# Kernel tuning notes

Hardware: AMD Instinct MI355X
Metric: run time of the kernel (lower is better)

Reference implementation:

```python
import jax, jax.numpy as jnp
import numpy as np

ALPHA = 0.2  # LeakyReLU negative slope
MASK_VAL = -9e15


def setup_inputs() -> dict:
    key = jax.random.key(0)
    k1, k2, k3, k4 = jax.random.split(key, 4)
    B, N, F_IN = 4, 2048, 256
    H, HD = 8, 32  # out_features = H*HD = 256
    x = jax.random.normal(k1, (B, N, F_IN), dtype=jnp.float32)
    adj = jax.random.randint(k2, (B, N, N), 0, 2, dtype=jnp.int32)
    W = jax.random.normal(k3, (H, F_IN, HD), dtype=jnp.float32) * (1.0 / np.sqrt(F_IN))
    a = jax.random.normal(k4, (H, 2 * HD, 1), dtype=jnp.float32) * 0.1
    return {"x": x, "adj": adj, "W": W, "a": a}


def reference(x, adj, W, a):
    # x: (B,N,F), W: (H,F,D), a: (H,2D,1)
    B, N, _ = x.shape
    H, _, D = W.shape
    Wh = jnp.einsum('bnf,hfd->bhnd', x, W)  # (B,H,N,D)
    # Split additive attention vector: cat([Wh_i, Wh_j]) @ a == Wh_i@a1 + Wh_j@a2
    a1 = a[:, :D, 0]   # (H,D)
    a2 = a[:, D:, 0]   # (H,D)
    s1 = jnp.einsum('bhnd,hd->bhn', Wh, a1)  # source scores
    s2 = jnp.einsum('bhnd,hd->bhn', Wh, a2)  # target scores
    e = jax.nn.leaky_relu(s1[:, :, :, None] + s2[:, :, None, :], negative_slope=ALPHA)  # (B,H,N,N)
    e = jnp.where(adj[:, None, :, :] == 0, MASK_VAL, e)
    attention = jax.nn.softmax(e, axis=-1)  # dropout skipped (eval mode)
    h = jnp.einsum('bhij,bhjd->bhid', attention, Wh)  # (B,H,N,D)
    h = jnp.transpose(h, (0, 2, 1, 3)).reshape(B, N, H * D)
    return jax.nn.elu(h)
```

## Files before the change

### kernel.cpp

```cpp
#include <hip/hip_runtime.h>
#include <hip/hip_bf16.h>

#define ALPHA 0.2f

typedef __attribute__((ext_vector_type(8))) short short8;
typedef __attribute__((ext_vector_type(8))) _Float16 h8;
typedef __attribute__((ext_vector_type(2))) _Float16 h2v;
typedef __attribute__((ext_vector_type(4))) float f32x4;

static constexpr int B = 4, N = 2048, F = 256, H = 8, D = 32;
static constexpr int SZ_X = B * N * F, SZ_ADJ = B * N * N, SZ_W = H * F * D, SZ_A = H * 2 * D;
static const float C1 = 1.4426950408889634f;
static const float C2 = ALPHA * 1.4426950408889634f;


__device__ __forceinline__ unsigned rne16(unsigned u) {
    return u + 0x7fffu + ((u >> 16) & 1u);
}
__device__ __forceinline__ unsigned pk_rne(float a, float b) {
    return __builtin_amdgcn_perm(rne16(__float_as_uint(b)),
                                 rne16(__float_as_uint(a)), 0x07060302u);
}
__device__ __forceinline__ unsigned h2mul(unsigned a, unsigned b) {
    h2v r = __builtin_bit_cast(h2v, a) * __builtin_bit_cast(h2v, b);
    return __builtin_bit_cast(unsigned, r);
}
__device__ __forceinline__ unsigned h2max(unsigned a, unsigned b) {
    h2v r = __builtin_elementwise_max(__builtin_bit_cast(h2v, a),
                                      __builtin_bit_cast(h2v, b));
    return __builtin_bit_cast(unsigned, r);
}

__global__ void k0_prep(const float* __restrict__ Wp, const float* __restrict__ ap,
                        unsigned short* __restrict__ WTbf, float* __restrict__ AF) {
    int bid = blockIdx.x;
    int h = bid >> 5, d = bid & 31;
    int f = threadIdx.x;
    WTbf[(h * D + d) * F + f] =
        (unsigned short)(rne16(__float_as_uint(Wp[(h * F + f) * D + d])) >> 16);
    if (d == 0 && f < 64) AF[h * 64 + f] = ap[h * 64 + f];
}

__global__ void kbit(const int* __restrict__ adj, unsigned long long* __restrict__ bm) {
    int wid = blockIdx.x * 4 + (threadIdx.x >> 6);
    int lane = threadIdx.x & 63;
    size_t base = (size_t)wid * 16;
#pragma unroll
    for (int s = 0; s < 16; s++) {
        size_t strip = base + s;
        int v = adj[strip * 64 + lane];
        unsigned long long m = __ballot(v != 0);
        if (lane == 0) bm[strip] = m;
    }
}

__global__ __launch_bounds__(256) void k12(const float* __restrict__ x,
                                           const unsigned short* __restrict__ WTbf,
                                           const float* __restrict__ AF,
                                           unsigned short* __restrict__ WHT,
                                           float* __restrict__ S1,
                                           _Float16* __restrict__ UH,
                                           _Float16* __restrict__ VH) {
    __shared__ unsigned short XA[16 * 264];
    __shared__ unsigned short WB[256 * 40];
    int bid = blockIdx.x;
    int b = bid >> 7;
    int n0 = (bid & 127) * 16;
    int t = threadIdx.x;
    int wave = t >> 6, lane = t & 63;
    int lm = lane & 15, lq = lane >> 4;

#pragma unroll
    for (int q = 0; q < 4; q++) {
        int idx = q * 256 + t;
        int row = idx >> 6, c16 = idx & 63;
        f32x4 v = *(const f32x4*)(x + (size_t)(b * N + n0 + row) * F + c16 * 4);
        unsigned* dst = (unsigned*)&XA[row * 264 + c16 * 4];
        dst[0] = pk_rne(v[0], v[1]);
        dst[1] = pk_rne(v[2], v[3]);
    }

    f32x4 acc[4] = {};
    for (int kc = 0; kc < 8; kc++) {
        __syncthreads();
#pragma unroll
        for (int q = 0; q < 4; q++) {
            int idx = q * 256 + t;
            int row = idx >> 2, c = idx & 3;
            short8 w = *(const short8*)(WTbf + row * 256 + kc * 32 + c * 8);
            *(short8*)&WB[row * 40 + c * 8] = w;
        }
        __syncthreads();
        short8 afr = *(const short8*)&XA[lm * 264 + kc * 32 + lq * 8];
#pragma unroll
        for (int c = 0; c < 4; c++) {
            short8 bfr = *(const short8*)&WB[(wave * 64 + c * 16 + lm) * 40 + lq * 8];
            acc[c] = __builtin_amdgcn_mfma_f32_16x16x32_bf16(afr, bfr, acc[c], 0, 0, 0);
        }
    }

#pragma unroll
    for (int c = 0; c < 4; c++) {
        int hd = wave * 64 + c * 16 + lm;
        unsigned short w0 = __builtin_bit_cast(unsigned short, (_Float16)acc[c][0]);
        unsigned short w1 = __builtin_bit_cast(unsigned short, (_Float16)acc[c][1]);
        unsigned short w2 = __builtin_bit_cast(unsigned short, (_Float16)acc[c][2]);
        unsigned short w3 = __builtin_bit_cast(unsigned short, (_Float16)acc[c][3]);
        uint2 pk;
        pk.x = (unsigned)w0 | ((unsigned)w1 << 16);
        pk.y = (unsigned)w2 | ((unsigned)w3 << 16);
        *(uint2*)&WHT[((size_t)b * 256 + hd) * 2048 + n0 + lq * 4] = pk;
    }
#pragma unroll
    for (int cp = 0; cp < 2; cp++) {
        int h = wave * 2 + cp;
        float a1l = AF[h * 64 + lm],      a1h = AF[h * 64 + 16 + lm];
        float a2l = AF[h * 64 + 32 + lm], a2h = AF[h * 64 + 48 + lm];
#pragma unroll
        for (int r = 0; r < 4; r++) {
            float s1p = acc[cp * 2][r] * a1l + acc[cp * 2 + 1][r] * a1h;
            float s2p = acc[cp * 2][r] * a2l + acc[cp * 2 + 1][r] * a2h;
#pragma unroll
            for (int off = 1; off <= 8; off <<= 1) {
                s1p += __shfl_xor(s1p, off);
                s2p += __shfl_xor(s2p, off);
            }
            if (lm == 0) {
                int bh = b * 8 + h, n = n0 + lq * 4 + r;
                S1[(size_t)bh * 2048 + n] = s1p;
                UH[(size_t)bh * 2048 + n] = (_Float16)exp2f(C1 * s2p);
                VH[(size_t)bh * 2048 + n] = (_Float16)exp2f(C2 * s2p);
            }
        }
    }
}

__global__ __launch_bounds__(512) void k3_attn(
    const unsigned* __restrict__ bm32,
    const unsigned short* __restrict__ WHT,
    const float* __restrict__ S1,
    const _Float16* __restrict__ UH, const _Float16* __restrict__ VH,
    float* __restrict__ out) {
    __shared__ unsigned short LW[256 * 136];
    __shared__ unsigned LM[16 * 66];
    __shared__ unsigned short LU[8 * 128];
    __shared__ unsigned short LV[8 * 128];

    int bid = blockIdx.x;
    int b = bid >> 7;
    int i0 = (bid & 127) * 16;
    int t = threadIdx.x;
    int wave = t >> 6, lane = t & 63;
    int h = wave;
    int bh = b * 8 + h;
    int irow = lane & 15, quad = lane >> 4;

    {
        int row = t >> 5, w0 = (t & 31) * 2;
        uint2 mv = *(const uint2*)(bm32 + ((size_t)(b * N + i0 + row)) * 64 + w0);
        LM[row * 66 + w0] = mv.x;
        LM[row * 66 + w0 + 1] = mv.y;
    }

    float s1i = S1[(size_t)bh * N + i0 + irow];
    unsigned short cw = __builtin_bit_cast(unsigned short, (_Float16)exp2f((C2 - C1) * s1i));
    unsigned ci2 = (unsigned)cw | ((unsigned)cw << 16);

    union { h8 v; unsigned u[4]; } ones;
    ones.u[0] = ones.u[1] = ones.u[2] = ones.u[3] = 0x3C003C00u;

    f32x4 acc0 = {0.f, 0.f, 0.f, 0.f};
    f32x4 acc1 = {0.f, 0.f, 0.f, 0.f};
    f32x4 accL = {0.f, 0.f, 0.f, 0.f};

    for (int cc = 0; cc < 16; cc++) {
        __syncthreads();
        const unsigned short* src = WHT + (size_t)b * 256 * 2048 + cc * 128;
#pragma unroll
        for (int q = 0; q < 8; q++) {
            int idx = q * 512 + t;
            int row = idx >> 4, u = idx & 15;
            short8 v = *(const short8*)(src + (size_t)row * 2048 + u * 8);
            *(short8*)&LW[row * 136 + u * 8] = v;
        }
        if (t < 256) {
            int which = t >> 7;
            int hh = (t & 127) >> 4, u16 = t & 15;
            const _Float16* s = (which ? VH : UH) + (size_t)(b * 8 + hh) * 2048 + cc * 128 + u16 * 8;
            short8 v = *(const short8*)s;
            unsigned short* dst = which ? LV : LU;
            *(short8*)&dst[hh * 128 + u16 * 8] = v;
        }
        __syncthreads();
#pragma unroll
        for (int g = 0; g < 4; g++) {
            unsigned mk = LM[irow * 66 + cc * 4 + g] >> (quad * 8);
            int jl = g * 32 + quad * 8;
            uint4 uw = *(const uint4*)&LU[h * 128 + jl];
            uint4 vw = *(const uint4*)&LV[h * 128 + jl];
            unsigned m0 = ((mk & 1u)   ? 0x3C00u : 0u) | ((mk & 2u)   ? 0x3C000000u : 0u);
            unsigned m1 = ((mk & 4u)   ? 0x3C00u : 0u) | ((mk & 8u)   ? 0x3C000000u : 0u);
            unsigned m2 = ((mk & 16u)  ? 0x3C00u : 0u) | ((mk & 32u)  ? 0x3C000000u : 0u);
            unsigned m3 = ((mk & 64u)  ? 0x3C00u : 0u) | ((mk & 128u) ? 0x3C000000u : 0u);
            union { h8 v; unsigned u[4]; } af;
            af.u[0] = h2mul(h2max(uw.x, h2mul(ci2, vw.x)), m0);
            af.u[1] = h2mul(h2max(uw.y, h2mul(ci2, vw.y)), m1);
            af.u[2] = h2mul(h2max(uw.z, h2mul(ci2, vw.z)), m2);
            af.u[3] = h2mul(h2max(uw.w, h2mul(ci2, vw.w)), m3);
            h8 bf0 = *(const h8*)&LW[(h * 32 + irow) * 136 + jl];
            h8 bf1 = *(const h8*)&LW[(h * 32 + 16 + irow) * 136 + jl];
            acc0 = __builtin_amdgcn_mfma_f32_16x16x32_f16(af.v, bf0, acc0, 0, 0, 0);
            acc1 = __builtin_amdgcn_mfma_f32_16x16x32_f16(af.v, bf1, acc1, 0, 0, 0);
            accL = __builtin_amdgcn_mfma_f32_16x16x32_f16(af.v, ones.v, accL, 0, 0, 0);
        }
    }
#pragma unroll
    for (int r = 0; r < 4; r++) {
        float lr = accL[r];
        float rin = 1.0f / (lr > 0.f ? lr : 1.f);
        float v0 = acc0[r] * rin;
        float v1 = acc1[r] * rin;
        v0 = v0 > 0.f ? v0 : __expf(v0) - 1.f;
        v1 = v1 > 0.f ? v1 : __expf(v1) - 1.f;
        size_t rowb = (size_t)(b * N + i0 + quad * 4 + r) * (H * D) + h * D;
        out[rowb + irow] = v0;
        out[rowb + 16 + irow] = v1;
    }
}

extern "C" void kernel_launch(void* const* d_in, const int* in_sizes, int n_in,
                              void* d_out, int out_size, void* d_ws, size_t ws_size,
                              hipStream_t stream) {
    const void *xP = nullptr, *adjP = nullptr, *WP = nullptr, *aP = nullptr;
    for (int i = 0; i < n_in; i++) {
        switch (in_sizes[i]) {
            case SZ_X:   xP = d_in[i]; break;
            case SZ_ADJ: adjP = d_in[i]; break;
            case SZ_W:   WP = d_in[i]; break;
            case SZ_A:   aP = d_in[i]; break;
            default: break;
        }
    }
    if (!xP || !adjP || !WP || !aP) { xP = d_in[0]; adjP = d_in[1]; WP = d_in[2]; aP = d_in[3]; }
    float* out = (float*)d_out;

    char* ws = (char*)d_ws;
    unsigned short* WTbf = (unsigned short*)(ws);
    float* AF  = (float*)(ws + 131072);
    float* S1  = (float*)(ws + 133120);
    _Float16* UH = (_Float16*)(ws + 395264);
    _Float16* VH = (_Float16*)(ws + 526336);
    unsigned short* WHT = (unsigned short*)(ws + 657408);
    unsigned long long* BM = (unsigned long long*)(ws + 4851712);

    k0_prep<<<256, 256, 0, stream>>>((const float*)WP, (const float*)aP, WTbf, AF);
    kbit<<<4096, 256, 0, stream>>>((const int*)adjP, BM);
    k12<<<512, 256, 0, stream>>>((const float*)xP, WTbf, AF, WHT, S1, UH, VH);
    k3_attn<<<512, 512, 0, stream>>>((const unsigned*)BM, WHT, S1, UH, VH, out);
}
```

Measured before the change: 164.5 us.

## Fuse adjacency bitmask build into attention kernel and use per-wave private LDS tiles

Removes the separate kbit kernel: each attention block now reads its 16 adjacency rows directly and ballots them into an LDS bitmask, avoiding a kernel launch and the bitmask round trip through global memory. The attention loop no longer uses block-wide barriers. Each wave loads only its own head's 32 WHT rows into a private LDS slice, and U/V values are read straight from global memory. Without barriers, waves can drift apart and overlap loads with MFMA work. The cost is that the adjacency read is now serialized at block start with no overlap.

```diff
diff --git a/kernel.cpp b/kernel.cpp
--- a/kernel.cpp
+++ b/kernel.cpp
@@ -39,19 +39,6 @@
     WTbf[(h * D + d) * F + f] =
         (unsigned short)(rne16(__float_as_uint(Wp[(h * F + f) * D + d])) >> 16);
     if (d == 0 && f < 64) AF[h * 64 + f] = ap[h * 64 + f];
-}
-
-__global__ void kbit(const int* __restrict__ adj, unsigned long long* __restrict__ bm) {
-    int wid = blockIdx.x * 4 + (threadIdx.x >> 6);
-    int lane = threadIdx.x & 63;
-    size_t base = (size_t)wid * 16;
-#pragma unroll
-    for (int s = 0; s < 16; s++) {
-        size_t strip = base + s;
-        int v = adj[strip * 64 + lane];
-        unsigned long long m = __ballot(v != 0);
-        if (lane == 0) bm[strip] = m;
-    }
 }
 
 __global__ __launch_bounds__(256) void k12(const float* __restrict__ x,
@@ -136,15 +123,13 @@
 }
 
 __global__ __launch_bounds__(512) void k3_attn(
-    const unsigned* __restrict__ bm32,
+    const int* __restrict__ adj,
     const unsigned short* __restrict__ WHT,
     const float* __restrict__ S1,
     const _Float16* __restrict__ UH, const _Float16* __restrict__ VH,
     float* __restrict__ out) {
-    __shared__ unsigned short LW[256 * 136];
     __shared__ unsigned LM[16 * 66];
-    __shared__ unsigned short LU[8 * 128];
-    __shared__ unsigned short LV[8 * 128];
+    __shared__ unsigned short LW[8 * 32 * 136];
 
     int bid = blockIdx.x;
     int b = bid >> 7;
@@ -155,12 +140,21 @@
     int bh = b * 8 + h;
     int irow = lane & 15, quad = lane >> 4;
 
-    {
-        int row = t >> 5, w0 = (t & 31) * 2;
-        uint2 mv = *(const uint2*)(bm32 + ((size_t)(b * N + i0 + row)) * 64 + w0);
-        LM[row * 66 + w0] = mv.x;
-        LM[row * 66 + w0 + 1] = mv.y;
-    }
+#pragma unroll
+    for (int rr = 0; rr < 2; rr++) {
+        int row = wave * 2 + rr;
+        const int* arow = adj + ((size_t)(b * N + i0 + row)) * N;
+#pragma unroll 4
+        for (int w64 = 0; w64 < 32; w64++) {
+            int v = arow[w64 * 64 + lane];
+            unsigned long long m = __ballot(v != 0);
+            if (lane == 0) {
+                LM[row * 66 + w64 * 2]     = (unsigned)m;
+                LM[row * 66 + w64 * 2 + 1] = (unsigned)(m >> 32);
+            }
+        }
+    }
+    __syncthreads();
 
     float s1i = S1[(size_t)bh * N + i0 + irow];
     unsigned short cw = __builtin_bit_cast(unsigned short, (_Float16)exp2f((C2 - C1) * s1i));
@@ -169,35 +163,29 @@
     union { h8 v; unsigned u[4]; } ones;
     ones.u[0] = ones.u[1] = ones.u[2] = ones.u[3] = 0x3C003C00u;
 
+    unsigned short* lw = LW + wave * (32 * 136);
+    const unsigned short* wsrc = WHT + ((size_t)b * 256 + h * 32) * 2048;
+    const _Float16* up = UH + (size_t)bh * 2048;
+    const _Float16* vp = VH + (size_t)bh * 2048;
+
     f32x4 acc0 = {0.f, 0.f, 0.f, 0.f};
     f32x4 acc1 = {0.f, 0.f, 0.f, 0.f};
     f32x4 accL = {0.f, 0.f, 0.f, 0.f};
 
     for (int cc = 0; cc < 16; cc++) {
-        __syncthreads();
-        const unsigned short* src = WHT + (size_t)b * 256 * 2048 + cc * 128;
-#pragma unroll
-        for (int q = 0; q < 8; q++) {
-            int idx = q * 512 + t;
-            int row = idx >> 4, u = idx & 15;
-            short8 v = *(const short8*)(src + (size_t)row * 2048 + u * 8);
-            *(short8*)&LW[row * 136 + u * 8] = v;
-        }
-        if (t < 256) {
-            int which = t >> 7;
-            int hh = (t & 127) >> 4, u16 = t & 15;
-            const _Float16* s = (which ? VH : UH) + (size_t)(b * 8 + hh) * 2048 + cc * 128 + u16 * 8;
-            short8 v = *(const short8*)s;
-            unsigned short* dst = which ? LV : LU;
-            *(short8*)&dst[hh * 128 + u16 * 8] = v;
-        }
-        __syncthreads();
+#pragma unroll
+        for (int k = 0; k < 8; k++) {
+            int unit = k * 64 + lane;
+            int row = unit >> 4, u16 = unit & 15;
+            short8 v = *(const short8*)(wsrc + (size_t)row * 2048 + cc * 128 + u16 * 8);
+            *(short8*)&lw[row * 136 + u16 * 8] = v;
+        }
 #pragma unroll
         for (int g = 0; g < 4; g++) {
             unsigned mk = LM[irow * 66 + cc * 4 + g] >> (quad * 8);
             int jl = g * 32 + quad * 8;
-            uint4 uw = *(const uint4*)&LU[h * 128 + jl];
-            uint4 vw = *(const uint4*)&LV[h * 128 + jl];
+            uint4 uw = *(const uint4*)(up + cc * 128 + jl);
+            uint4 vw = *(const uint4*)(vp + cc * 128 + jl);
             unsigned m0 = ((mk & 1u)   ? 0x3C00u : 0u) | ((mk & 2u)   ? 0x3C000000u : 0u);
             unsigned m1 = ((mk & 4u)   ? 0x3C00u : 0u) | ((mk & 8u)   ? 0x3C000000u : 0u);
             unsigned m2 = ((mk & 16u)  ? 0x3C00u : 0u) | ((mk & 32u)  ? 0x3C000000u : 0u);
@@ -207,8 +195,8 @@
             af.u[1] = h2mul(h2max(uw.y, h2mul(ci2, vw.y)), m1);
             af.u[2] = h2mul(h2max(uw.z, h2mul(ci2, vw.z)), m2);
             af.u[3] = h2mul(h2max(uw.w, h2mul(ci2, vw.w)), m3);
-            h8 bf0 = *(const h8*)&LW[(h * 32 + irow) * 136 + jl];
-            h8 bf1 = *(const h8*)&LW[(h * 32 + 16 + irow) * 136 + jl];
+            h8 bf0 = *(const h8*)&lw[irow * 136 + jl];
+            h8 bf1 = *(const h8*)&lw[(16 + irow) * 136 + jl];
             acc0 = __builtin_amdgcn_mfma_f32_16x16x32_f16(af.v, bf0, acc0, 0, 0, 0);
             acc1 = __builtin_amdgcn_mfma_f32_16x16x32_f16(af.v, bf1, acc1, 0, 0, 0);
             accL = __builtin_amdgcn_mfma_f32_16x16x32_f16(af.v, ones.v, accL, 0, 0, 0);
@@ -251,10 +239,8 @@
     _Float16* UH = (_Float16*)(ws + 395264);
     _Float16* VH = (_Float16*)(ws + 526336);
     unsigned short* WHT = (unsigned short*)(ws + 657408);
-    unsigned long long* BM = (unsigned long long*)(ws + 4851712);
 
     k0_prep<<<256, 256, 0, stream>>>((const float*)WP, (const float*)aP, WTbf, AF);
-    kbit<<<4096, 256, 0, stream>>>((const int*)adjP, BM);
     k12<<<512, 256, 0, stream>>>((const float*)xP, WTbf, AF, WHT, S1, UH, VH);
-    k3_attn<<<512, 512, 0, stream>>>((const unsigned*)BM, WHT, S1, UH, VH, out);
-}
+    k3_attn<<<512, 512, 0, stream>>>((const int*)adjP, WHT, S1, UH, VH, out);
+}
```

Result: slower. 173.6 us (+5.5%).

## Remap attention blocks per head with double-buffered Wh tiles; stream W directly

Applied to the files above, without the earlier changes.

The attention kernel now gives each block one (batch, head) pair and 128 query rows, four waves of 32 rows each, instead of all 8 heads over 16 rows. Each block stages only that head's 32 Wh rows in shared memory. That tile is double-buffered with register prefetch, so there is one barrier per chunk instead of two. The U/V factors are read straight from global memory rather than staged. The projection kernel drops its shared-memory W staging and reads a re-laid-out bf16 W directly from global/L2, removing 16 barriers. The trade-off is less reuse of the adjacency mask per block, with the mask for 128 rows loaded per head, plus uncached global reads for U/V in the inner loop.

```diff
diff --git a/kernel.cpp b/kernel.cpp
--- a/kernel.cpp
+++ b/kernel.cpp
@@ -4,6 +4,7 @@
 #define ALPHA 0.2f
 
 typedef __attribute__((ext_vector_type(8))) short short8;
+typedef __attribute__((ext_vector_type(4))) short s4;
 typedef __attribute__((ext_vector_type(8))) _Float16 h8;
 typedef __attribute__((ext_vector_type(2))) _Float16 h2v;
 typedef __attribute__((ext_vector_type(4))) float f32x4;
@@ -30,14 +31,18 @@
                                       __builtin_bit_cast(h2v, b));
     return __builtin_bit_cast(unsigned, r);
 }
+__device__ __forceinline__ unsigned dup16f(float x) {
+    unsigned short w = __builtin_bit_cast(unsigned short, (_Float16)x);
+    return (unsigned)w | ((unsigned)w << 16);
+}
 
 __global__ void k0_prep(const float* __restrict__ Wp, const float* __restrict__ ap,
-                        unsigned short* __restrict__ WTbf, float* __restrict__ AF) {
+                        unsigned short* __restrict__ WT2, float* __restrict__ AF) {
     int bid = blockIdx.x;
     int h = bid >> 5, d = bid & 31;
     int f = threadIdx.x;
-    WTbf[(h * D + d) * F + f] =
-        (unsigned short)(rne16(__float_as_uint(Wp[(h * F + f) * D + d])) >> 16);
+    unsigned short v = (unsigned short)(rne16(__float_as_uint(Wp[(h * F + f) * D + d])) >> 16);
+    WT2[(size_t)(f >> 5) * 8192 + (h * 32 + d) * 32 + (f & 31)] = v;
     if (d == 0 && f < 64) AF[h * 64 + f] = ap[h * 64 + f];
 }
 
@@ -55,14 +60,13 @@
 }
 
 __global__ __launch_bounds__(256) void k12(const float* __restrict__ x,
-                                           const unsigned short* __restrict__ WTbf,
+                                           const unsigned short* __restrict__ WT2,
                                            const float* __restrict__ AF,
                                            unsigned short* __restrict__ WHT,
                                            float* __restrict__ S1,
                                            _Float16* __restrict__ UH,
                                            _Float16* __restrict__ VH) {
     __shared__ unsigned short XA[16 * 264];
-    __shared__ unsigned short WB[256 * 40];
     int bid = blockIdx.x;
     int b = bid >> 7;
     int n0 = (bid & 127) * 16;
@@ -79,22 +83,16 @@
         dst[0] = pk_rne(v[0], v[1]);
         dst[1] = pk_rne(v[2], v[3]);
     }
+    __syncthreads();
 
     f32x4 acc[4] = {};
+#pragma unroll
     for (int kc = 0; kc < 8; kc++) {
-        __syncthreads();
-#pragma unroll
-        for (int q = 0; q < 4; q++) {
-            int idx = q * 256 + t;
-            int row = idx >> 2, c = idx & 3;
-            short8 w = *(const short8*)(WTbf + row * 256 + kc * 32 + c * 8);
-            *(short8*)&WB[row * 40 + c * 8] = w;
-        }
-        __syncthreads();
         short8 afr = *(const short8*)&XA[lm * 264 + kc * 32 + lq * 8];
 #pragma unroll
         for (int c = 0; c < 4; c++) {
-            short8 bfr = *(const short8*)&WB[(wave * 64 + c * 16 + lm) * 40 + lq * 8];
+            int hd = wave * 64 + c * 16 + lm;
+            short8 bfr = *(const short8*)(WT2 + (size_t)kc * 8192 + hd * 32 + lq * 8);
             acc[c] = __builtin_amdgcn_mfma_f32_16x16x32_bf16(afr, bfr, acc[c], 0, 0, 0);
         }
     }
@@ -135,96 +133,134 @@
     }
 }
 
-__global__ __launch_bounds__(512) void k3_attn(
+__global__ __launch_bounds__(256) void k3_attn(
     const unsigned* __restrict__ bm32,
     const unsigned short* __restrict__ WHT,
     const float* __restrict__ S1,
     const _Float16* __restrict__ UH, const _Float16* __restrict__ VH,
     float* __restrict__ out) {
-    __shared__ unsigned short LW[256 * 136];
-    __shared__ unsigned LM[16 * 66];
-    __shared__ unsigned short LU[8 * 128];
-    __shared__ unsigned short LV[8 * 128];
+    __shared__ unsigned LM[4][32 * 66];
+    __shared__ unsigned short LW[2][32 * 140];
 
     int bid = blockIdx.x;
-    int b = bid >> 7;
-    int i0 = (bid & 127) * 16;
+    int isup = bid & 15;
+    int bh = bid >> 4;
+    int b = bh >> 3, h = bh & 7;
+    int i0 = isup * 128;
     int t = threadIdx.x;
     int wave = t >> 6, lane = t & 63;
-    int h = wave;
-    int bh = b * 8 + h;
     int irow = lane & 15, quad = lane >> 4;
+    int iw = i0 + wave * 32;
 
     {
-        int row = t >> 5, w0 = (t & 31) * 2;
-        uint2 mv = *(const uint2*)(bm32 + ((size_t)(b * N + i0 + row)) * 64 + w0);
-        LM[row * 66 + w0] = mv.x;
-        LM[row * 66 + w0 + 1] = mv.y;
-    }
-
-    float s1i = S1[(size_t)bh * N + i0 + irow];
-    unsigned short cw = __builtin_bit_cast(unsigned short, (_Float16)exp2f((C2 - C1) * s1i));
-    unsigned ci2 = (unsigned)cw | ((unsigned)cw << 16);
+        unsigned* lm = LM[wave];
+        const unsigned* src = bm32 + ((size_t)(b * N + iw)) * 64;
+#pragma unroll 4
+        for (int r = 0; r < 32; r++)
+            lm[r * 66 + lane] = src[(size_t)r * 64 + lane];
+    }
+
+    const unsigned short* wsrc = WHT + ((size_t)b * 256 + h * 32) * 2048;
+    int srow = t >> 3, sseg = (t & 7) * 16;
+
+    {
+        const unsigned short* g = wsrc + (size_t)srow * 2048 + sseg;
+        union { short8 v; s4 q[2]; } a, c;
+        a.v = *(const short8*)(g);
+        c.v = *(const short8*)(g + 8);
+        unsigned short* d = &LW[0][srow * 140 + sseg];
+        *(s4*)(d) = a.q[0]; *(s4*)(d + 4) = a.q[1];
+        *(s4*)(d + 8) = c.q[0]; *(s4*)(d + 12) = c.q[1];
+    }
+
+    float s1A = S1[(size_t)bh * 2048 + iw + irow];
+    float s1B = S1[(size_t)bh * 2048 + iw + 16 + irow];
+    unsigned ci2A = dup16f(exp2f((C2 - C1) * s1A));
+    unsigned ci2B = dup16f(exp2f((C2 - C1) * s1B));
+    const _Float16* up = UH + (size_t)bh * 2048;
+    const _Float16* vp = VH + (size_t)bh * 2048;
 
     union { h8 v; unsigned u[4]; } ones;
     ones.u[0] = ones.u[1] = ones.u[2] = ones.u[3] = 0x3C003C00u;
 
-    f32x4 acc0 = {0.f, 0.f, 0.f, 0.f};
-    f32x4 acc1 = {0.f, 0.f, 0.f, 0.f};
-    f32x4 accL = {0.f, 0.f, 0.f, 0.f};
+    f32x4 aA0 = {0,0,0,0}, aA1 = {0,0,0,0}, aAL = {0,0,0,0};
+    f32x4 aB0 = {0,0,0,0}, aB1 = {0,0,0,0}, aBL = {0,0,0,0};
+    __syncthreads();
 
     for (int cc = 0; cc < 16; cc++) {
+        union { short8 v; s4 q[2]; } pa, pc;
+        if (cc < 15) {
+            const unsigned short* g = wsrc + (size_t)srow * 2048 + (cc + 1) * 128 + sseg;
+            pa.v = *(const short8*)(g);
+            pc.v = *(const short8*)(g + 8);
+        }
+        const unsigned short* lwp = LW[cc & 1];
+        const unsigned* lmw = LM[wave];
+#pragma unroll
+        for (int ks = 0; ks < 4; ks++) {
+            int jl = ks * 32 + quad * 8;
+            int jg = cc * 128 + jl;
+            uint4 uw = *(const uint4*)(up + jg);
+            uint4 vw = *(const uint4*)(vp + jg);
+            unsigned mkA = lmw[irow * 66 + cc * 4 + ks] >> (quad * 8);
+            unsigned mkB = lmw[(16 + irow) * 66 + cc * 4 + ks] >> (quad * 8);
+            unsigned mA0 = ((mkA & 1u)  ? 0x3C00u : 0u) | ((mkA & 2u)   ? 0x3C000000u : 0u);
+            unsigned mA1 = ((mkA & 4u)  ? 0x3C00u : 0u) | ((mkA & 8u)   ? 0x3C000000u : 0u);
+            unsigned mA2 = ((mkA & 16u) ? 0x3C00u : 0u) | ((mkA & 32u)  ? 0x3C000000u : 0u);
+            unsigned mA3 = ((mkA & 64u) ? 0x3C00u : 0u) | ((mkA & 128u) ? 0x3C000000u : 0u);
+            unsigned mB0 = ((mkB & 1u)  ? 0x3C00u : 0u) | ((mkB & 2u)   ? 0x3C000000u : 0u);
+            unsigned mB1 = ((mkB & 4u)  ? 0x3C00u : 0u) | ((mkB & 8u)   ? 0x3C000000u : 0u);
+            unsigned mB2 = ((mkB & 16u) ? 0x3C00u : 0u) | ((mkB & 32u)  ? 0x3C000000u : 0u);
+            unsigned mB3 = ((mkB & 64u) ? 0x3C00u : 0u) | ((mkB & 128u) ? 0x3C000000u : 0u);
+            union { h8 v; unsigned u[4]; } afA, afB;
+            afA.u[0] = h2mul(h2max(uw.x, h2mul(ci2A, vw.x)), mA0);
+            afA.u[1] = h2mul(h2max(uw.y, h2mul(ci2A, vw.y)), mA1);
+            afA.u[2] = h2mul(h2max(uw.z, h2mul(ci2A, vw.z)), mA2);
+            afA.u[3] = h2mul(h2max(uw.w, h2mul(ci2A, vw.w)), mA3);
+            afB.u[0] = h2mul(h2max(uw.x, h2mul(ci2B, vw.x)), mB0);
+            afB.u[1] = h2mul(h2max(uw.y, h2mul(ci2B, vw.y)), mB1);
+            afB.u[2] = h2mul(h2max(uw.z, h2mul(ci2B, vw.z)), mB2);
+            afB.u[3] = h2mul(h2max(uw.w, h2mul(ci2B, vw.w)), mB3);
+            union { short8 v; s4 q[2]; } bf0, bf1;
+            bf0.q[0] = *(const s4*)&lwp[irow * 140 + jl];
+            bf0.q[1] = *(const s4*)&lwp[irow * 140 + jl + 4];
+            bf1.q[0] = *(const s4*)&lwp[(16 + irow) * 140 + jl];
+            bf1.q[1] = *(const s4*)&lwp[(16 + irow) * 140 + jl + 4];
+            h8 b0 = __builtin_bit_cast(h8, bf0.v);
+            h8 b1 = __builtin_bit_cast(h8, bf1.v);
+            aA0 = __builtin_amdgcn_mfma_f32_16x16x32_f16(afA.v, b0, aA0, 0, 0, 0);
+            aA1 = __builtin_amdgcn_mfma_f32_16x16x32_f16(afA.v, b1, aA1, 0, 0, 0);
+            aAL = __builtin_amdgcn_mfma_f32_16x16x32_f16(afA.v, ones.v, aAL, 0, 0, 0);
+            aB0 = __builtin_amdgcn_mfma_f32_16x16x32_f16(afB.v, b0, aB0, 0, 0, 0);
+            aB1 = __builtin_amdgcn_mfma_f32_16x16x32_f16(afB.v, b1, aB1, 0, 0, 0);
+            aBL = __builtin_amdgcn_mfma_f32_16x16x32_f16(afB.v, ones.v, aBL, 0, 0, 0);
+        }
+        if (cc < 15) {
+            unsigned short* d = &LW[(cc + 1) & 1][srow * 140 + sseg];
+            *(s4*)(d) = pa.q[0]; *(s4*)(d + 4) = pa.q[1];
+            *(s4*)(d + 8) = pc.q[0]; *(s4*)(d + 12) = pc.q[1];
+        }
         __syncthreads();
-        const unsigned short* src = WHT + (size_t)b * 256 * 2048 + cc * 128;
-#pragma unroll
-        for (int q = 0; q < 8; q++) {
-            int idx = q * 512 + t;
-            int row = idx >> 4, u = idx & 15;
-            short8 v = *(const short8*)(src + (size_t)row * 2048 + u * 8);
-            *(short8*)&LW[row * 136 + u * 8] = v;
-        }
-        if (t < 256) {
-            int which = t >> 7;
-            int hh = (t & 127) >> 4, u16 = t & 15;
-            const _Float16* s = (which ? VH : UH) + (size_t)(b * 8 + hh) * 2048 + cc * 128 + u16 * 8;
-            short8 v = *(const short8*)s;
-            unsigned short* dst = which ? LV : LU;
-            *(short8*)&dst[hh * 128 + u16 * 8] = v;
-        }
-        __syncthreads();
-#pragma unroll
-        for (int g = 0; g < 4; g++) {
-            unsigned mk = LM[irow * 66 + cc * 4 + g] >> (quad * 8);
-            int jl = g * 32 + quad * 8;
-            uint4 uw = *(const uint4*)&LU[h * 128 + jl];
-            uint4 vw = *(const uint4*)&LV[h * 128 + jl];
-            unsigned m0 = ((mk & 1u)   ? 0x3C00u : 0u) | ((mk & 2u)   ? 0x3C000000u : 0u);
-            unsigned m1 = ((mk & 4u)   ? 0x3C00u : 0u) | ((mk & 8u)   ? 0x3C000000u : 0u);
-            unsigned m2 = ((mk & 16u)  ? 0x3C00u : 0u) | ((mk & 32u)  ? 0x3C000000u : 0u);
-            unsigned m3 = ((mk & 64u)  ? 0x3C00u : 0u) | ((mk & 128u) ? 0x3C000000u : 0u);
-            union { h8 v; unsigned u[4]; } af;
-            af.u[0] = h2mul(h2max(uw.x, h2mul(ci2, vw.x)), m0);
-            af.u[1] = h2mul(h2max(uw.y, h2mul(ci2, vw.y)), m1);
-            af.u[2] = h2mul(h2max(uw.z, h2mul(ci2, vw.z)), m2);
-            af.u[3] = h2mul(h2max(uw.w, h2mul(ci2, vw.w)), m3);
-            h8 bf0 = *(const h8*)&LW[(h * 32 + irow) * 136 + jl];
-            h8 bf1 = *(const h8*)&LW[(h * 32 + 16 + irow) * 136 + jl];
-            acc0 = __builtin_amdgcn_mfma_f32_16x16x32_f16(af.v, bf0, acc0, 0, 0, 0);
-            acc1 = __builtin_amdgcn_mfma_f32_16x16x32_f16(af.v, bf1, acc1, 0, 0, 0);
-            accL = __builtin_amdgcn_mfma_f32_16x16x32_f16(af.v, ones.v, accL, 0, 0, 0);
-        }
-    }
+    }
+
 #pragma unroll
     for (int r = 0; r < 4; r++) {
-        float lr = accL[r];
-        float rin = 1.0f / (lr > 0.f ? lr : 1.f);
-        float v0 = acc0[r] * rin;
-        float v1 = acc1[r] * rin;
-        v0 = v0 > 0.f ? v0 : __expf(v0) - 1.f;
-        v1 = v1 > 0.f ? v1 : __expf(v1) - 1.f;
-        size_t rowb = (size_t)(b * N + i0 + quad * 4 + r) * (H * D) + h * D;
-        out[rowb + irow] = v0;
-        out[rowb + 16 + irow] = v1;
+        float lA = aAL[r], lB = aBL[r];
+        float rA = 1.0f / (lA > 0.f ? lA : 1.f);
+        float rB = 1.0f / (lB > 0.f ? lB : 1.f);
+        float vA0 = aA0[r] * rA, vA1 = aA1[r] * rA;
+        float vB0 = aB0[r] * rB, vB1 = aB1[r] * rB;
+        vA0 = vA0 > 0.f ? vA0 : __expf(vA0) - 1.f;
+        vA1 = vA1 > 0.f ? vA1 : __expf(vA1) - 1.f;
+        vB0 = vB0 > 0.f ? vB0 : __expf(vB0) - 1.f;
+        vB1 = vB1 > 0.f ? vB1 : __expf(vB1) - 1.f;
+        int iA = iw + quad * 4 + r, iB = iA + 16;
+        size_t rbA = (size_t)(b * N + iA) * 256 + h * 32;
+        size_t rbB = (size_t)(b * N + iB) * 256 + h * 32;
+        out[rbA + irow] = vA0;
+        out[rbA + 16 + irow] = vA1;
+        out[rbB + irow] = vB0;
+        out[rbB + 16 + irow] = vB1;
     }
 }
 
@@ -245,7 +281,7 @@
     float* out = (float*)d_out;
 
     char* ws = (char*)d_ws;
-    unsigned short* WTbf = (unsigned short*)(ws);
+    unsigned short* WT2 = (unsigned short*)(ws);
     float* AF  = (float*)(ws + 131072);
     float* S1  = (float*)(ws + 133120);
     _Float16* UH = (_Float16*)(ws + 395264);
@@ -253,8 +289,8 @@
     unsigned short* WHT = (unsigned short*)(ws + 657408);
     unsigned long long* BM = (unsigned long long*)(ws + 4851712);
 
-    k0_prep<<<256, 256, 0, stream>>>((const float*)WP, (const float*)aP, WTbf, AF);
+    k0_prep<<<256, 256, 0, stream>>>((const float*)WP, (const float*)aP, WT2, AF);
     kbit<<<4096, 256, 0, stream>>>((const int*)adjP, BM);
-    k12<<<512, 256, 0, stream>>>((const float*)xP, WTbf, AF, WHT, S1, UH, VH);
-    k3_attn<<<512, 512, 0, stream>>>((const unsigned*)BM, WHT, S1, UH, VH, out);
-}
+    k12<<<512, 256, 0, stream>>>((const float*)xP, WT2, AF, WHT, S1, UH, VH);
+    k3_attn<<<512, 256, 0, stream>>>((const unsigned*)BM, WHT, S1, UH, VH, out);
+}
```

Measured after the change: 157.6 us. 4.2% less time.
